# Optimization experiments

Hardware: AMD Instinct MI355X
Metric: run time of the kernel (lower is better)

The kernel has to match this reference:

```python
import jax, jax.numpy as jnp
import numpy as np

W = 32  # voxel grid resolution, codebook size = W**3 = 32768


def _grid_points(w=W):
    # meshgrid of integer voxel indices, shape (3, w, w, w), then map to cell
    # centers in [-1, 1]: ((idx + 0.5) * 2 / w - 1), flattened to (w^3, 3).
    idx = np.stack(np.meshgrid(np.arange(w), np.arange(w), np.arange(w), indexing='ij'))
    pts = (idx + 0.5) * 2.0 / w - 1.0
    return jnp.asarray(pts.reshape(3, -1).T, dtype=jnp.float32)  # (32768, 3)


def setup_inputs() -> dict:
    key = jax.random.key(0)
    B, N = 4, 1024
    # points uniform in [-1, 1]^3
    x = jax.random.uniform(key, (B, N, 3), dtype=jnp.float32) * 2.0 - 1.0
    return {"x": x, "grid_points": _grid_points()}


def reference(x, grid_points):
    B, N, _ = x.shape
    K = grid_points.shape[0]  # 32768
    flat_x = x.reshape(B * N, 3)
    dists = (jnp.sum(flat_x ** 2, axis=1, keepdims=True)
             + jnp.sum(grid_points ** 2, axis=1)
             - 2.0 * flat_x @ grid_points.T)
    enc = jnp.argmin(dists, axis=1).reshape(B, N)
    enc = jnp.sort(enc, axis=1)  # (B, N) int
    # scatter ones into the occupied voxels (duplicates just re-set to 1)
    voxel = jnp.zeros((B, K), dtype=jnp.float32)
    voxel = voxel.at[jnp.arange(B)[:, None], enc].set(1.0)
    voxel = voxel.reshape(B, 1, W, W, W)
    voxel = (voxel - 0.5) / 0.5 * 0.8  # map {0,1} -> {-0.8, 0.8}
    return enc, voxel
```

## Files before the change

### kernel.cpp

```cpp
#include <hip/hip_runtime.h>


#define VW 32
#define VK (VW*VW*VW)
#define NPTS 1024
#define NB 4
#define NWORDS (VK/32)

#define BARRIER_LDS() asm volatile("s_waitcnt lgkmcnt(0)\n\ts_barrier" ::: "memory")

__device__ __forceinline__ int cmpex_shfl(int v, int jj, int k, int t) {
    int pv = __shfl_xor(v, jj);
    bool keepmin = (((t & jj) == 0) == ((t & k) == 0));
    return keepmin ? min(v, pv) : max(v, pv);
}

__global__ __launch_bounds__(NPTS) void pq_kernel(const float* __restrict__ x,
                                                  float* __restrict__ out) {
    const int b = blockIdx.x;
    const int t = threadIdx.x;

    float* enc_out = out;
    float* vox = out + NB * NPTS + (size_t)b * VK;

    __shared__ unsigned bm[NWORDS];
    __shared__ int sb[2][NPTS];

    bm[t] = 0u;

    const float* p = x + (size_t)(b * NPTS + t) * 3;
    float px = p[0], py = p[1], pz = p[2];
    int i = min(max((int)floorf((px + 1.0f) * 16.0f), 0), VW - 1);
    int j = min(max((int)floorf((py + 1.0f) * 16.0f), 0), VW - 1);
    int l = min(max((int)floorf((pz + 1.0f) * 16.0f), 0), VW - 1);
    int v = i * (VW * VW) + j * VW + l;

    BARRIER_LDS();
    atomicOr(&bm[v >> 5], 1u << (v & 31));
    BARRIER_LDS();

    float4* v4 = (float4*)vox;
    #pragma unroll
    for (int g = 0; g < 8; ++g) {
        int m = g * NPTS + t;
        unsigned nib = bm[m >> 3] >> ((m & 7) * 4);
        float4 f;
        f.x = (nib & 1u) ? 0.8f : -0.8f;
        f.y = (nib & 2u) ? 0.8f : -0.8f;
        f.z = (nib & 4u) ? 0.8f : -0.8f;
        f.w = (nib & 8u) ? 0.8f : -0.8f;
        v4[m] = f;
    }

    #pragma unroll
    for (int k = 2; k <= 64; k <<= 1)
        #pragma unroll
        for (int jj = k >> 1; jj > 0; jj >>= 1)
            v = cmpex_shfl(v, jj, k, t);

    int cur = 0;
    sb[0][t] = v;
    BARRIER_LDS();

    #pragma unroll
    for (int k = 128; k <= NPTS; k <<= 1) {
        for (int jj = k >> 1; jj >= 64; jj >>= 1) {
            int pv = sb[cur][t ^ jj];
            bool keepmin = (((t & jj) == 0) == ((t & k) == 0));
            v = keepmin ? min(v, pv) : max(v, pv);
            sb[cur ^ 1][t] = v;
            BARRIER_LDS();
            cur ^= 1;
        }
        #pragma unroll
        for (int jj = 32; jj > 0; jj >>= 1)
            v = cmpex_shfl(v, jj, k, t);
        if (k < NPTS) {
            sb[cur ^ 1][t] = v;
            BARRIER_LDS();
            cur ^= 1;
        }
    }

    enc_out[b * NPTS + t] = (float)v;
}

extern "C" void kernel_launch(void* const* d_in, const int* in_sizes, int n_in,
                              void* d_out, int out_size, void* d_ws, size_t ws_size,
                              hipStream_t stream) {
    const float* x = (const float*)d_in[0];
    float* out = (float*)d_out;

    pq_kernel<<<NB, NPTS, 0, stream>>>(x, out);
}
```

Measured before the change: 10.78 us.

## Replace cross-wave bitonic merge with rank-by-binary-search merge sort

Each wave now sorts its 64 values with shuffle-based bitonic sort, writes them to shared memory once, and every thread then computes its global rank by binary searching the other 15 sorted runs, scattering its value directly to the output. This removes the many LDS barrier stages of the bitonic merge across waves. In exchange, each thread does 15 binary searches of about seven LDS reads each. The per-wave sort is also moved ahead of the bitmap barrier so it overlaps with that wait.

```diff
diff --git a/kernel.cpp b/kernel.cpp
--- a/kernel.cpp
+++ b/kernel.cpp
@@ -9,22 +9,18 @@
 
 #define BARRIER_LDS() asm volatile("s_waitcnt lgkmcnt(0)\n\ts_barrier" ::: "memory")
 
-__device__ __forceinline__ int cmpex_shfl(int v, int jj, int k, int t) {
-    int pv = __shfl_xor(v, jj);
-    bool keepmin = (((t & jj) == 0) == ((t & k) == 0));
-    return keepmin ? min(v, pv) : max(v, pv);
-}
-
 __global__ __launch_bounds__(NPTS) void pq_kernel(const float* __restrict__ x,
                                                   float* __restrict__ out) {
     const int b = blockIdx.x;
     const int t = threadIdx.x;
+    const int lane = t & 63;
+    const int wave = t >> 6;
 
-    float* enc_out = out;
+    float* enc_out = out + b * NPTS;
     float* vox = out + NB * NPTS + (size_t)b * VK;
 
     __shared__ unsigned bm[NWORDS];
-    __shared__ int sb[2][NPTS];
+    __shared__ int sb[NPTS];
 
     bm[t] = 0u;
 
@@ -37,6 +33,18 @@
 
     BARRIER_LDS();
     atomicOr(&bm[v >> 5], 1u << (v & 31));
+
+    #pragma unroll
+    for (int k = 2; k <= 64; k <<= 1) {
+        #pragma unroll
+        for (int jj = k >> 1; jj > 0; jj >>= 1) {
+            int pv = __shfl_xor(v, jj);
+            bool keepmin = (((lane & jj) == 0) == ((lane & k) == 0));
+            v = keepmin ? min(v, pv) : max(v, pv);
+        }
+    }
+
+    sb[t] = v;
     BARRIER_LDS();
 
     float4* v4 = (float4*)vox;
@@ -52,37 +60,25 @@
         v4[m] = f;
     }
 
+    int rank = lane;
     #pragma unroll
-    for (int k = 2; k <= 64; k <<= 1)
+    for (int s = 0; s < 16; ++s) {
+        if (s == wave) continue;
+        const int* run = &sb[s * 64];
+        const bool le = (s < wave);
+        int pos = 0;
         #pragma unroll
-        for (int jj = k >> 1; jj > 0; jj >>= 1)
-            v = cmpex_shfl(v, jj, k, t);
-
-    int cur = 0;
-    sb[0][t] = v;
-    BARRIER_LDS();
-
-    #pragma unroll
-    for (int k = 128; k <= NPTS; k <<= 1) {
-        for (int jj = k >> 1; jj >= 64; jj >>= 1) {
-            int pv = sb[cur][t ^ jj];
-            bool keepmin = (((t & jj) == 0) == ((t & k) == 0));
-            v = keepmin ? min(v, pv) : max(v, pv);
-            sb[cur ^ 1][t] = v;
-            BARRIER_LDS();
-            cur ^= 1;
+        for (int w = 32; w >= 1; w >>= 1) {
+            int c = run[pos + w - 1];
+            bool take = le ? (c <= v) : (c < v);
+            pos += take ? w : 0;
         }
-        #pragma unroll
-        for (int jj = 32; jj > 0; jj >>= 1)
-            v = cmpex_shfl(v, jj, k, t);
-        if (k < NPTS) {
-            sb[cur ^ 1][t] = v;
-            BARRIER_LDS();
-            cur ^= 1;
-        }
+        int c = run[pos < 63 ? pos : 63];
+        pos += (le ? (c <= v) : (c < v)) && (pos == 63);
+        rank += pos;
     }
 
-    enc_out[b * NPTS + t] = (float)v;
+    enc_out[rank] = (float)v;
 }
 
 extern "C" void kernel_launch(void* const* d_in, const int* in_sizes, int n_in,
```

Result: slower. 16.04 us (+48.8%).
